# Optimization experiments

Hardware: AMD Instinct MI355X
Metric: run time of the kernel (lower is better)

## Reference

```python
import jax, jax.numpy as jnp
import numpy as np
import math

N_HEADS = 16
DIM = 1024

def setup_inputs() -> dict:
    key = jax.random.key(0)
    ks = jax.random.split(key, 10)
    B, S, D = 4, 2048, DIM
    xavier = math.sqrt(2.0 / (D + D))  # xavier_normal_ std for square weight
    query = jax.random.normal(ks[0], (B, S, D), dtype=jnp.float32)
    mask = jnp.ones((B, S), dtype=jnp.int32)
    Wq = jax.random.normal(ks[1], (D, D), dtype=jnp.float32) * xavier
    Wk = jax.random.normal(ks[2], (D, D), dtype=jnp.float32) * xavier
    Wv = jax.random.normal(ks[3], (D, D), dtype=jnp.float32) * xavier
    Wo = jax.random.normal(ks[4], (D, D), dtype=jnp.float32) * xavier
    bound = 1.0 / math.sqrt(D)  # default nn.Linear bias init U(-1/sqrt(fan_in), ...)
    bq = jax.random.uniform(ks[5], (D,), jnp.float32, -bound, bound)
    bk = jax.random.uniform(ks[6], (D,), jnp.float32, -bound, bound)
    bv = jax.random.uniform(ks[7], (D,), jnp.float32, -bound, bound)
    bo = jax.random.uniform(ks[8], (D,), jnp.float32, -bound, bound)
    return {"query": query, "mask": mask, "Wq": Wq, "bq": bq, "Wk": Wk, "bk": bk,
            "Wv": Wv, "bv": bv, "Wo": Wo, "bo": bo}

def reference(query, mask, Wq, bq, Wk, bk, Wv, bv, Wo, bo):
    B, S, D = query.shape
    H = N_HEADS
    Dh = D // H
    scale = math.sqrt(Dh)
    def heads(x):  # [B,S,D] -> [B,H,S,Dh]
        return x.reshape(B, S, H, Dh).transpose(0, 2, 1, 3)
    q = heads(query @ Wq.T + bq)
    k = heads(query @ Wk.T + bk)
    v = heads(query @ Wv.T + bv)
    scores = jnp.einsum('bhsd,bhtd->bhst', q, k)  # [B,H,S,S]
    keep = (mask != 0)[:, None, None, :]  # [B,1,1,S]
    scores = jnp.where(keep, scores, jnp.float32(-1e20))
    attn = jax.nn.softmax(scores / scale, axis=-1)
    ctx = jnp.einsum('bhst,bhtd->bhsd', attn, v)  # [B,H,S,Dh]
    ctx = ctx.transpose(0, 2, 1, 3).reshape(B, S, D)
    return ctx @ Wo.T + bo
```

## Files before the change

### kernel.cpp

```cpp
#include <hip/hip_runtime.h>

typedef unsigned short u16;
typedef unsigned int u32;
typedef __attribute__((ext_vector_type(8))) short short8;
typedef __attribute__((ext_vector_type(8))) __bf16 bf16x8;
typedef __attribute__((ext_vector_type(4))) float f32x4;
typedef __attribute__((ext_vector_type(2))) u32 u32x2;

__device__ __forceinline__ float bf2f(u16 u) { return __uint_as_float(((u32)u) << 16); }
__device__ __forceinline__ u16 f2bf(float f) {
  u32 u = __float_as_uint(f);
  u = (u + 0x7fffu + ((u >> 16) & 1u)) >> 16;
  return (u16)u;
}

__device__ __forceinline__ float EXP2(float x) {
#if __has_builtin(__builtin_amdgcn_exp2f)
  return __builtin_amdgcn_exp2f(x);
#else
  return exp2f(x);
#endif
}

__device__ __forceinline__ u32 CVTPK(float lo, float hi) {
  u32 r;
  asm("v_cvt_pk_bf16_f32 %0, %1, %2" : "=v"(r) : "v"(lo), "v"(hi));
  return r;
}

template <typename V>
__device__ __forceinline__ auto mfma_try(V a, V b, f32x4 c, int)
    -> decltype(__builtin_amdgcn_mfma_f32_16x16x32_bf16(a, b, c, 0, 0, 0)) {
  return __builtin_amdgcn_mfma_f32_16x16x32_bf16(a, b, c, 0, 0, 0);
}
template <typename V>
__device__ __forceinline__ f32x4 mfma_try(V a, V b, f32x4 c, long) {
  return __builtin_amdgcn_mfma_f32_16x16x32_bf16(
      __builtin_bit_cast(bf16x8, a), __builtin_bit_cast(bf16x8, b), c, 0, 0, 0);
}
__device__ __forceinline__ f32x4 MFMA(short8 a, short8 b, f32x4 c) {
  return mfma_try(a, b, c, 0);
}

#define GLOAD16(gsrc, ldst)                                                  \
  __builtin_amdgcn_global_load_lds(                                          \
      (const __attribute__((address_space(1))) void*)(gsrc),                 \
      (__attribute__((address_space(3))) void*)(ldst), 16, 0, 0)

#define SQ 2048
#define NH 16
#define DH 64
#define DMODEL 1024

__global__ void detect_dtype(const u16* __restrict__ q, int* __restrict__ flag) {
  __shared__ int cnt;
  if (threadIdx.x == 0) cnt = 0;
  __syncthreads();
  const int k = threadIdx.x * 16384 + 128;
  const u16 u = q[2 * k];
  const int e = (u >> 7) & 0xFF;
  if (e >= 96 && e <= 143) atomicAdd(&cnt, 1);
  __syncthreads();
  if (threadIdx.x == 0) *flag = (cnt < 128) ? 1 : 0;
}

__device__ __forceinline__ short8 cvt8_f32(const float* s) {
  f32x4 a = *(const f32x4*)s;
  f32x4 b = *(const f32x4*)(s + 4);
  short8 o;
#pragma unroll
  for (int j = 0; j < 4; ++j) o[j] = (short)f2bf(a[j]);
#pragma unroll
  for (int j = 0; j < 4; ++j) o[4 + j] = (short)f2bf(b[j]);
  return o;
}

__global__ void cvt_tensor(const void* __restrict__ src, u16* __restrict__ dst,
                           int n8, const int* __restrict__ flag) {
  const bool isf32 = (*flag != 0);
  int i = blockIdx.x * blockDim.x + threadIdx.x;
  const int stride = gridDim.x * blockDim.x;
  if (isf32) {
    const float* s = (const float*)src;
    for (; i < n8; i += stride) *(short8*)(dst + i * 8) = cvt8_f32(s + i * 8);
  } else {
    const short8* s = (const short8*)src;
    for (; i < n8; i += stride) *(short8*)(dst + i * 8) = s[i];
  }
}

__global__ void cvt_w4(const void* s0, const void* s1, const void* s2, const void* s3,
                       u16* __restrict__ dst, const int* __restrict__ flag) {
  const bool isf32 = (*flag != 0);
  int i = blockIdx.x * blockDim.x + threadIdx.x;
  const int stride = gridDim.x * blockDim.x;
  for (; i < (1 << 19); i += stride) {
    const int seg = i >> 17, off = i & ((1 << 17) - 1);
    const void* s = (seg == 0) ? s0 : (seg == 1) ? s1 : (seg == 2) ? s2 : s3;
    u16* d = dst + ((long)seg << 20) + (long)off * 8;
    if (isf32) *(short8*)d = cvt8_f32((const float*)s + off * 8);
    else *(short8*)d = *((const short8*)s + off);
  }
}

__global__ void cvt_b4(const void* s0, const void* s1, const void* s2, const void* s3,
                       u16* __restrict__ dst, const int* __restrict__ flag) {
  const bool isf32 = (*flag != 0);
  int i = blockIdx.x * blockDim.x + threadIdx.x;
  if (i >= 512) return;
  const int seg = i >> 7, off = i & 127;
  const void* s = (seg == 0) ? s0 : (seg == 1) ? s1 : (seg == 2) ? s2 : s3;
  u16* d = dst + seg * 1024 + off * 8;
  if (isf32) *(short8*)d = cvt8_f32((const float*)s + off * 8);
  else *(short8*)d = *((const short8*)s + off);
}

__global__ __launch_bounds__(256, 2) void gemm_qkv(
    const u16* __restrict__ A, const u16* __restrict__ W,
    const u16* __restrict__ bias, u16* __restrict__ qb,
    u16* __restrict__ kb, u16* __restrict__ vT) {
  __shared__ __align__(16) u16 As[128 * 32];
  __shared__ __align__(16) u16 Bs[128 * 32];
  const int tid = threadIdx.x;
  const int lane = tid & 63;
  const int wv = tid >> 6;
  const int wr = wv >> 1, wc = wv & 1;
  const int K = DMODEL;

  const int nwg = gridDim.x;
  const int cpx = nwg >> 3;
  const int bid = (blockIdx.x % 8) * cpx + (blockIdx.x >> 3);

  const int tm = bid / 24, tn = bid % 24;
  const int m0 = tm << 7, n0 = tn << 7;

  f32x4 acc[4][4];
#pragma unroll
  for (int i = 0; i < 4; ++i)
#pragma unroll
    for (int j = 0; j < 4; ++j)
#pragma unroll
      for (int r = 0; r < 4; ++r) acc[i][j][r] = 0.f;

  const int srow = tid >> 2;
  const int skk = (tid & 3) * 8;
  const u16* a0 = A + (long)(m0 + srow) * K + skk;
  const u16* a1 = A + (long)(m0 + 64 + srow) * K + skk;
  const u16* b0 = W + (long)(n0 + srow) * K + skk;
  const u16* b1 = W + (long)(n0 + 64 + srow) * K + skk;
  u16* lA0 = &As[tid * 8];
  u16* lA1 = &As[(256 + tid) * 8];
  u16* lB0 = &Bs[tid * 8];
  u16* lB1 = &Bs[(256 + tid) * 8];

  const int rk = 8 * (lane >> 4);
  const int rrow = lane & 15;
  const int r0 = (lane >> 4) * 4;

  for (int k0 = 0; k0 < K; k0 += 32) {
    GLOAD16(a0 + k0, lA0);
    GLOAD16(a1 + k0, lA1);
    GLOAD16(b0 + k0, lB0);
    GLOAD16(b1 + k0, lB1);
    asm volatile("s_waitcnt vmcnt(0)" ::: "memory");
    __syncthreads();
    short8 af[4], bf[4];
#pragma unroll
    for (int mi = 0; mi < 4; ++mi)
      af[mi] = *(const short8*)&As[(wr * 64 + mi * 16 + rrow) * 32 + rk];
#pragma unroll
    for (int ni = 0; ni < 4; ++ni)
      bf[ni] = *(const short8*)&Bs[(wc * 64 + ni * 16 + rrow) * 32 + rk];
#pragma unroll
    for (int mi = 0; mi < 4; ++mi)
#pragma unroll
      for (int ni = 0; ni < 4; ++ni)
        acc[mi][ni] = MFMA(af[mi], bf[ni], acc[mi][ni]);
    __syncthreads();
  }

  const int seg = n0 >> 10;
  const int nbase = n0 & 1023;
  u16* dst = (seg == 0) ? qb : (seg == 1) ? kb : vT;
#pragma unroll
  for (int ni = 0; ni < 4; ++ni) {
    const int col = n0 + wc * 64 + ni * 16 + rrow;
    const float bv = bf2f(bias[col]);
    const int cl = nbase + wc * 64 + ni * 16 + rrow;
    const int h = cl >> 6, dh = cl & 63;
#pragma unroll
    for (int mi = 0; mi < 4; ++mi) {
#pragma unroll
      for (int r = 0; r < 4; ++r) {
        const int row = m0 + wr * 64 + mi * 16 + r0 + r;
        const float v = acc[mi][ni][r] + bv;
        const int b = row >> 11, s = row & 2047;
        if (seg < 2) {
          dst[(((long)(b * NH + h) * SQ) + s) * DH + dh] = f2bf(v);
        } else {
          dst[(((long)(b * NH + h) * DH) + dh) * SQ + s] = f2bf(v);
        }
      }
    }
  }
}

__global__ __launch_bounds__(256, 2) void gemm_out(
    const u16* __restrict__ A, const u16* __restrict__ W,
    const u16* __restrict__ bias, void* __restrict__ Cv,
    const int* __restrict__ flag, int M, int N, int K) {
  __shared__ __align__(16) u16 As[128 * 32];
  __shared__ __align__(16) u16 Bs[128 * 32];
  const int tid = threadIdx.x;
  const int lane = tid & 63;
  const int wv = tid >> 6;
  const int wr = wv >> 1, wc = wv & 1;
  const bool isf32 = (*flag != 0);

  const int nwg = gridDim.x;
  const int cpx = nwg >> 3;
  const int bid = (blockIdx.x % 8) * cpx + (blockIdx.x >> 3);

  const int tiles_n = N >> 7;
  const int tm = bid / tiles_n, tn = bid % tiles_n;
  const int m0 = tm << 7, n0 = tn << 7;

  f32x4 acc[4][4];
#pragma unroll
  for (int i = 0; i < 4; ++i)
#pragma unroll
    for (int j = 0; j < 4; ++j)
#pragma unroll
      for (int r = 0; r < 4; ++r) acc[i][j][r] = 0.f;

  const int srow = tid >> 2;
  const int skk = (tid & 3) * 8;
  const u16* a0 = A + (long)(m0 + srow) * K + skk;
  const u16* a1 = A + (long)(m0 + 64 + srow) * K + skk;
  const u16* b0 = W + (long)(n0 + srow) * K + skk;
  const u16* b1 = W + (long)(n0 + 64 + srow) * K + skk;
  u16* lA0 = &As[tid * 8];
  u16* lA1 = &As[(256 + tid) * 8];
  u16* lB0 = &Bs[tid * 8];
  u16* lB1 = &Bs[(256 + tid) * 8];

  const int rk = 8 * (lane >> 4);
  const int rrow = lane & 15;
  const int r0 = (lane >> 4) * 4;

  for (int k0 = 0; k0 < K; k0 += 32) {
    GLOAD16(a0 + k0, lA0);
    GLOAD16(a1 + k0, lA1);
    GLOAD16(b0 + k0, lB0);
    GLOAD16(b1 + k0, lB1);
    asm volatile("s_waitcnt vmcnt(0)" ::: "memory");
    __syncthreads();
    short8 af[4], bf[4];
#pragma unroll
    for (int mi = 0; mi < 4; ++mi)
      af[mi] = *(const short8*)&As[(wr * 64 + mi * 16 + rrow) * 32 + rk];
#pragma unroll
    for (int ni = 0; ni < 4; ++ni)
      bf[ni] = *(const short8*)&Bs[(wc * 64 + ni * 16 + rrow) * 32 + rk];
#pragma unroll
    for (int mi = 0; mi < 4; ++mi)
#pragma unroll
      for (int ni = 0; ni < 4; ++ni)
        acc[mi][ni] = MFMA(af[mi], bf[ni], acc[mi][ni]);
    __syncthreads();
  }

#pragma unroll
  for (int ni = 0; ni < 4; ++ni) {
    const int col = n0 + wc * 64 + ni * 16 + rrow;
    const float bv = bf2f(bias[col]);
#pragma unroll
    for (int mi = 0; mi < 4; ++mi) {
#pragma unroll
      for (int r = 0; r < 4; ++r) {
        const int row = m0 + wr * 64 + mi * 16 + r0 + r;
        const float v = acc[mi][ni][r] + bv;
        const long idx = (long)row * N + col;
        if (isf32) ((float*)Cv)[idx] = v;
        else ((u16*)Cv)[idx] = f2bf(v);
      }
    }
  }
}

#define KVB 128
#define LSTR 72
#define LSTRV 136
#define LSTRP 68
#define SM_C 0.18033688011112043f

__global__ __launch_bounds__(256, 2) void attn_kernel(
    const u16* __restrict__ q, const u16* __restrict__ k,
    const u16* __restrict__ vT, const int* __restrict__ mask,
    u16* __restrict__ ctx) {
  __shared__ __align__(16) u16 Ks[KVB * LSTR];
  __shared__ __align__(16) u16 Vs[64 * LSTRV];
  __shared__ __align__(16) u16 Ps[4][32 * LSTRP];
  __shared__ __align__(16) float Msf[KVB];

  const int tid = threadIdx.x, lane = tid & 63, wv = tid >> 6;
  const int bh = blockIdx.y, b = bh >> 4, h = bh & 15;
  const int q0 = blockIdx.x * 128 + wv * 32;
  const u16* qb = q + (long)bh * SQ * DH;
  const u16* kb = k + (long)bh * SQ * DH;
  const u16* vb = vT + (long)bh * DH * SQ;
  const int g1 = lane >> 4;
  const int rq = lane & 15;
  const int rk = 8 * g1;
  const int r0 = 4 * g1;

  short8 aq[2][2];
#pragma unroll
  for (int m = 0; m < 2; ++m)
#pragma unroll
    for (int ks = 0; ks < 2; ++ks)
      aq[m][ks] = *(const short8*)&qb[(long)(q0 + m * 16 + rq) * DH + ks * 32 + rk];

  f32x4 oacc[2][4];
  float mrow[2], lrow[2];
#pragma unroll
  for (int m = 0; m < 2; ++m) {
    mrow[m] = -1.0e9f;
    lrow[m] = 0.f;
#pragma unroll
    for (int nf = 0; nf < 4; ++nf)
#pragma unroll
      for (int r = 0; r < 4; ++r) oacc[m][nf][r] = 0.f;
  }

  const int stg_r = tid >> 3;
  const int stg_c = (tid & 7) * 8;
  const int vr = tid >> 4;
  const int vc = (tid & 15) * 8;

  for (int t0 = 0; t0 < SQ; t0 += KVB) {
    short8 kvr[4], vvr[4];
#pragma unroll
    for (int j = 0; j < 4; ++j)
      kvr[j] = *(const short8*)&kb[(long)(t0 + stg_r + 32 * j) * DH + stg_c];
#pragma unroll
    for (int j = 0; j < 4; ++j)
      vvr[j] = *(const short8*)&vb[(long)(vr + 16 * j) * SQ + t0 + vc];
    float mv = 0.f;
    if (tid < KVB) mv = (mask[b * SQ + t0 + tid] != 0) ? 0.f : -1.0e9f;

    __syncthreads();
#pragma unroll
    for (int j = 0; j < 4; ++j)
      *(short8*)&Ks[(stg_r + 32 * j) * LSTR + stg_c] = kvr[j];
#pragma unroll
    for (int j = 0; j < 4; ++j)
      *(short8*)&Vs[(vr + 16 * j) * LSTRV + vc] = vvr[j];
    if (tid < KVB) Msf[tid] = mv;
    __syncthreads();

    f32x4 sacc[2][8];
#pragma unroll
    for (int f = 0; f < 8; ++f) {
      const short8 k0 = *(const short8*)&Ks[(f * 16 + rq) * LSTR + rk];
      const short8 k1 = *(const short8*)&Ks[(f * 16 + rq) * LSTR + 32 + rk];
      f32x4 z;
#pragma unroll
      for (int r = 0; r < 4; ++r) z[r] = 0.f;
#pragma unroll
      for (int m = 0; m < 2; ++m) {
        f32x4 t = MFMA(k0, aq[m][0], z);
        sacc[m][f] = MFMA(k1, aq[m][1], t);
      }
    }

#pragma unroll
    for (int f = 0; f < 8; ++f) {
      const f32x4 mo = *(const f32x4*)&Msf[f * 16 + 4 * g1];
#pragma unroll
      for (int m = 0; m < 2; ++m)
#pragma unroll
        for (int r = 0; r < 4; ++r)
          sacc[m][f][r] = __builtin_fmaf(sacc[m][f][r], SM_C, mo[r]);
    }

#pragma unroll
    for (int m = 0; m < 2; ++m) {
      f32x4 t4 = sacc[m][0];
#pragma unroll
      for (int f = 1; f < 8; ++f)
#pragma unroll
        for (int r = 0; r < 4; ++r) t4[r] = fmaxf(t4[r], sacc[m][f][r]);
      float vmax = fmaxf(fmaxf(t4[0], t4[1]), fmaxf(t4[2], t4[3]));
      vmax = fmaxf(vmax, __shfl_xor(vmax, 16));
      vmax = fmaxf(vmax, __shfl_xor(vmax, 32));

      const float mnew = fmaxf(mrow[m], vmax);
      const float sc = EXP2(mrow[m] - mnew);
      mrow[m] = mnew;

#pragma unroll
      for (int f = 0; f < 8; ++f)
#pragma unroll
        for (int r = 0; r < 4; ++r)
          sacc[m][f][r] = EXP2(sacc[m][f][r] - mnew);
      f32x4 s4;
#pragma unroll
      for (int r = 0; r < 4; ++r)
        s4[r] = ((sacc[m][0][r] + sacc[m][1][r]) + (sacc[m][2][r] + sacc[m][3][r])) +
                ((sacc[m][4][r] + sacc[m][5][r]) + (sacc[m][6][r] + sacc[m][7][r]));
      float tsum = (s4[0] + s4[1]) + (s4[2] + s4[3]);
      tsum += __shfl_xor(tsum, 16);
      tsum += __shfl_xor(tsum, 32);
      lrow[m] = lrow[m] * sc + tsum;

      f32x4 scr;
#pragma unroll
      for (int r = 0; r < 4; ++r) scr[r] = __shfl(sc, 4 * g1 + r);
#pragma unroll
      for (int nf = 0; nf < 4; ++nf)
#pragma unroll
        for (int r = 0; r < 4; ++r) oacc[m][nf][r] *= scr[r];
    }

#pragma unroll
    for (int half = 0; half < 2; ++half) {
#pragma unroll
      for (int m = 0; m < 2; ++m)
#pragma unroll
        for (int fl = 0; fl < 4; ++fl) {
          const int f = half * 4 + fl;
          u32x2 w;
          w[0] = CVTPK(sacc[m][f][0], sacc[m][f][1]);
          w[1] = CVTPK(sacc[m][f][2], sacc[m][f][3]);
          *(u32x2*)&Ps[wv][(m * 16 + rq) * LSTRP + fl * 16 + 4 * g1] = w;
        }
#pragma unroll
      for (int k2 = 0; k2 < 2; ++k2) {
        const int ks2 = half * 2 + k2;
        short8 pa[2];
#pragma unroll
        for (int m = 0; m < 2; ++m)
          pa[m] = *(const short8*)&Ps[wv][(m * 16 + rq) * LSTRP + k2 * 32 + rk];
#pragma unroll
        for (int nf = 0; nf < 4; ++nf) {
          const short8 bvv = *(const short8*)&Vs[(nf * 16 + rq) * LSTRV + ks2 * 32 + rk];
#pragma unroll
          for (int m = 0; m < 2; ++m)
            oacc[m][nf] = MFMA(pa[m], bvv, oacc[m][nf]);
        }
      }
    }
  }

#pragma unroll
  for (int m = 0; m < 2; ++m) {
    const float inv = 1.0f / lrow[m];
    f32x4 invr;
#pragma unroll
    for (int r = 0; r < 4; ++r) invr[r] = __shfl(inv, 4 * g1 + r);
#pragma unroll
    for (int nf = 0; nf < 4; ++nf)
#pragma unroll
      for (int r = 0; r < 4; ++r) {
        const int s = q0 + m * 16 + r0 + r;
        const int dh = nf * 16 + rq;
        ctx[(((long)(b * SQ + s)) * NH + h) * DH + dh] = f2bf(oacc[m][nf][r] * invr[r]);
      }
  }
}

extern "C" void kernel_launch(void* const* d_in, const int* in_sizes, int n_in,
                              void* d_out, int out_size, void* d_ws, size_t ws_size,
                              hipStream_t stream) {
  const void* query = d_in[0];
  const int* mask = (const int*)d_in[1];
  const void* Wq = d_in[2];
  const void* bq = d_in[3];
  const void* Wk = d_in[4];
  const void* bk = d_in[5];
  const void* Wv = d_in[6];
  const void* bv = d_in[7];
  const void* Wo = d_in[8];
  const void* bo = d_in[9];

  char* w = (char*)d_ws;
  int* flag = (int*)w;
  u16* qc = (u16*)(w + 256);
  u16* Wc = qc + (long)8388608;
  u16* bc = Wc + (long)4 * 1048576;
  u16* qh = bc + 4096;
  u16* kh = qh + (long)8388608;
  u16* vT = kh + (long)8388608;
  u16* ctx = vT + (long)8388608;

  dim3 blk(256);

  detect_dtype<<<1, 256, 0, stream>>>((const u16*)query, flag);
  cvt_tensor<<<2048, 256, 0, stream>>>(query, qc, 8388608 / 8, flag);
  cvt_w4<<<2048, 256, 0, stream>>>(Wq, Wk, Wv, Wo, Wc, flag);
  cvt_b4<<<2, 256, 0, stream>>>(bq, bk, bv, bo, bc, flag);

  const int M = 4 * SQ;

  gemm_qkv<<<dim3(1536), blk, 0, stream>>>(qc, Wc, bc, qh, kh, vT);

  dim3 attn_grid(SQ / 128, 64);
  attn_kernel<<<attn_grid, blk, 0, stream>>>(qh, kh, vT, mask, ctx);

  gemm_out<<<dim3((M / 128) * (DMODEL / 128)), blk, 0, stream>>>(
      ctx, Wc + 3 * 1048576, bc + 3072, d_out, flag, M, DMODEL, DMODEL);
}
```

Baseline: 349.4 us.

## Keep softmax probabilities in registers and remap blocks for XCD locality

The attention kernel no longer round-trips P through shared memory. The MFMA accumulator layout is packed directly into the A operand, and the V operand reads are permuted to match that k-ordering. Dropping the Ps buffer lowers LDS use, so the launch bound is raised to 3 blocks per CU. Both the QKV GEMM and the attention kernel also get an XCD-aware block index remapping, meant to keep tiles that share K/V or weight data on the same L2. The cost is possible register pressure from holding pa[2][4] under the tighter occupancy target.

```diff
diff --git a/kernel.cpp b/kernel.cpp
--- a/kernel.cpp
+++ b/kernel.cpp
@@ -26,6 +26,12 @@
   u32 r;
   asm("v_cvt_pk_bf16_f32 %0, %1, %2" : "=v"(r) : "v"(lo), "v"(hi));
   return r;
+}
+
+__device__ __forceinline__ short8 mk_s8(u32 a, u32 b, u32 c, u32 d) {
+  union { short8 s; u32 w[4]; } u;
+  u.w[0] = a; u.w[1] = b; u.w[2] = c; u.w[3] = d;
+  return u.s;
 }
 
 template <typename V>
@@ -127,11 +133,12 @@
   const int wr = wv >> 1, wc = wv & 1;
   const int K = DMODEL;
 
-  const int nwg = gridDim.x;
-  const int cpx = nwg >> 3;
-  const int bid = (blockIdx.x % 8) * cpx + (blockIdx.x >> 3);
-
-  const int tm = bid / 24, tn = bid % 24;
+  const int x = blockIdx.x & 7;
+  const int local = blockIdx.x >> 3;
+  const int sub = local >> 6;
+  const int within = local & 63;
+  const int tm = x * 8 + (within >> 3);
+  const int tn = sub * 8 + (within & 7);
   const int m0 = tm << 7, n0 = tn << 7;
 
   f32x4 acc[4][4];
@@ -291,21 +298,23 @@
 #define KVB 128
 #define LSTR 72
 #define LSTRV 136
-#define LSTRP 68
 #define SM_C 0.18033688011112043f
 
-__global__ __launch_bounds__(256, 2) void attn_kernel(
+__global__ __launch_bounds__(256, 3) void attn_kernel(
     const u16* __restrict__ q, const u16* __restrict__ k,
     const u16* __restrict__ vT, const int* __restrict__ mask,
     u16* __restrict__ ctx) {
   __shared__ __align__(16) u16 Ks[KVB * LSTR];
   __shared__ __align__(16) u16 Vs[64 * LSTRV];
-  __shared__ __align__(16) u16 Ps[4][32 * LSTRP];
   __shared__ __align__(16) float Msf[KVB];
 
   const int tid = threadIdx.x, lane = tid & 63, wv = tid >> 6;
-  const int bh = blockIdx.y, b = bh >> 4, h = bh & 15;
-  const int q0 = blockIdx.x * 128 + wv * 32;
+  const int xcd = blockIdx.x & 7;
+  const int local = blockIdx.x >> 3;
+  const int bh = xcd * 8 + (local >> 4);
+  const int qt = local & 15;
+  const int b = bh >> 4, h = bh & 15;
+  const int q0 = qt * 128 + wv * 32;
   const u16* qb = q + (long)bh * SQ * DH;
   const u16* kb = k + (long)bh * SQ * DH;
   const u16* vb = vT + (long)bh * DH * SQ;
@@ -384,6 +393,7 @@
           sacc[m][f][r] = __builtin_fmaf(sacc[m][f][r], SM_C, mo[r]);
     }
 
+    short8 pa[2][4];
 #pragma unroll
     for (int m = 0; m < 2; ++m) {
       f32x4 t4 = sacc[m][0];
@@ -421,34 +431,26 @@
       for (int nf = 0; nf < 4; ++nf)
 #pragma unroll
         for (int r = 0; r < 4; ++r) oacc[m][nf][r] *= scr[r];
+
+#pragma unroll
+      for (int ks2 = 0; ks2 < 4; ++ks2)
+        pa[m][ks2] = mk_s8(CVTPK(sacc[m][2 * ks2][0], sacc[m][2 * ks2][1]),
+                           CVTPK(sacc[m][2 * ks2][2], sacc[m][2 * ks2][3]),
+                           CVTPK(sacc[m][2 * ks2 + 1][0], sacc[m][2 * ks2 + 1][1]),
+                           CVTPK(sacc[m][2 * ks2 + 1][2], sacc[m][2 * ks2 + 1][3]));
     }
 
 #pragma unroll
-    for (int half = 0; half < 2; ++half) {
-#pragma unroll
-      for (int m = 0; m < 2; ++m)
-#pragma unroll
-        for (int fl = 0; fl < 4; ++fl) {
-          const int f = half * 4 + fl;
-          u32x2 w;
-          w[0] = CVTPK(sacc[m][f][0], sacc[m][f][1]);
-          w[1] = CVTPK(sacc[m][f][2], sacc[m][f][3]);
-          *(u32x2*)&Ps[wv][(m * 16 + rq) * LSTRP + fl * 16 + 4 * g1] = w;
-        }
-#pragma unroll
-      for (int k2 = 0; k2 < 2; ++k2) {
-        const int ks2 = half * 2 + k2;
-        short8 pa[2];
+    for (int ks2 = 0; ks2 < 4; ++ks2) {
+#pragma unroll
+      for (int nf = 0; nf < 4; ++nf) {
+        const int base = (nf * 16 + rq) * LSTRV + ks2 * 32 + 4 * g1;
+        const u32x2 lo = *(const u32x2*)&Vs[base];
+        const u32x2 hi = *(const u32x2*)&Vs[base + 16];
+        const short8 bvv = mk_s8(lo[0], lo[1], hi[0], hi[1]);
 #pragma unroll
         for (int m = 0; m < 2; ++m)
-          pa[m] = *(const short8*)&Ps[wv][(m * 16 + rq) * LSTRP + k2 * 32 + rk];
-#pragma unroll
-        for (int nf = 0; nf < 4; ++nf) {
-          const short8 bvv = *(const short8*)&Vs[(nf * 16 + rq) * LSTRV + ks2 * 32 + rk];
-#pragma unroll
-          for (int m = 0; m < 2; ++m)
-            oacc[m][nf] = MFMA(pa[m], bvv, oacc[m][nf]);
-        }
+          oacc[m][nf] = MFMA(pa[m][ks2], bvv, oacc[m][nf]);
       }
     }
   }
@@ -505,8 +507,7 @@
 
   gemm_qkv<<<dim3(1536), blk, 0, stream>>>(qc, Wc, bc, qh, kh, vT);
 
-  dim3 attn_grid(SQ / 128, 64);
-  attn_kernel<<<attn_grid, blk, 0, stream>>>(qh, kh, vT, mask, ctx);
+  attn_kernel<<<dim3(1024), blk, 0, stream>>>(qh, kh, vT, mask, ctx);
 
   gemm_out<<<dim3((M / 128) * (DMODEL / 128)), blk, 0, stream>>>(
       ctx, Wc + 3 * 1048576, bc + 3072, d_out, flag, M, DMODEL, DMODEL);
```

New measurement: 332.9 us. 4.7% less time.
